# Kernel tuning notes

Measured on AMD Instinct MI355X. Metric: run time of the kernel, lower is better.

The kernel has to match this reference:

```python
import jax, jax.numpy as jnp
import numpy as np
from jax import lax

DIM, HEADS, DIM_HEAD = 768, 12, 64
INNER = HEADS * DIM_HEAD
DIM_ROT = 32
FH = FW = 32
N = 1 + FH * FW
B = 8


def setup_inputs() -> dict:
    key = jax.random.key(0)
    ks = jax.random.split(key, 8)
    s = 0.02
    return {
        "x": jax.random.normal(ks[0], (B, N, DIM), jnp.float32),
        "sin": jax.random.normal(ks[1], (N - 1, DIM_ROT), jnp.float32),
        "cos": jax.random.normal(ks[2], (N - 1, DIM_ROT), jnp.float32),
        "ln_g": jnp.ones((DIM,), jnp.float32),
        "ln_b": jnp.zeros((DIM,), jnp.float32),
        "dw_w": jax.random.normal(ks[3], (DIM, 1, 5, 5), jnp.float32) * s,
        "pw_w": jax.random.normal(ks[4], (INNER, DIM, 1, 1), jnp.float32) * s,
        "kv_w": jax.random.normal(ks[5], (DIM, 2 * INNER), jnp.float32) * s,
        "out_w": jax.random.normal(ks[6], (INNER, DIM), jnp.float32) * s,
        "out_b": jnp.zeros((DIM,), jnp.float32),
        "fmap_h": FH,
        "fmap_w": FW,
    }


def _rotate_every_two(t):
    # (..., d) with pairs (x1, x2) -> (-x2, x1)
    shp = t.shape
    t = t.reshape(*shp[:-1], -1, 2)
    x1, x2 = t[..., 0], t[..., 1]
    return jnp.stack((-x2, x1), axis=-1).reshape(shp)


def _layernorm(x, g, b, eps=1e-5):
    mu = jnp.mean(x, -1, keepdims=True)
    var = jnp.var(x, -1, keepdims=True)
    return (x - mu) * lax.rsqrt(var + eps) * g + b


def reference(x, sin, cos, ln_g, ln_b, dw_w, pw_w, kv_w, out_w, out_b, fmap_h, fmap_w):
    b, n, _ = x.shape
    scale = DIM_HEAD ** -0.5
    xn = _layernorm(x, ln_g, ln_b)

    # --- query path: SpatialConv (depthwise 5x5 + 1x1), cls via Identity ---
    cls_tok, spatial = xn[:, :1], xn[:, 1:]
    fmap = spatial.reshape(b, fmap_h, fmap_w, DIM).transpose(0, 3, 1, 2)  # NCHW
    fmap = lax.conv_general_dilated(
        fmap, dw_w, window_strides=(1, 1), padding=[(2, 2), (2, 2)],
        dimension_numbers=("NCHW", "OIHW", "NCHW"), feature_group_count=DIM)
    fmap = lax.conv_general_dilated(
        fmap, pw_w, window_strides=(1, 1), padding="VALID",
        dimension_numbers=("NCHW", "OIHW", "NCHW"))
    q = fmap.transpose(0, 2, 3, 1).reshape(b, fmap_h * fmap_w, INNER)
    q = jnp.concatenate((cls_tok, q), axis=1)  # cls_proj is Identity (dim==inner)

    # --- kv projection ---
    kv = xn @ kv_w
    k, v = kv[..., :INNER], kv[..., INNER:]

    def to_heads(t):  # b n (h d) -> (b h) n d
        return t.reshape(b, n, HEADS, DIM_HEAD).transpose(0, 2, 1, 3).reshape(b * HEADS, n, DIM_HEAD)

    q, k, v = map(to_heads, (q, k, v))

    # --- partial rotary, skipping cls token ---
    def apply_rot(t):
        t_cls, t_sp = t[:, :1], t[:, 1:]
        t_rot, t_pass = t_sp[..., :DIM_ROT], t_sp[..., DIM_ROT:]
        t_rot = t_rot * cos + _rotate_every_two(t_rot) * sin
        return jnp.concatenate((t_cls, jnp.concatenate((t_rot, t_pass), -1)), axis=1)

    q, k = apply_rot(q), apply_rot(k)

    dots = jnp.einsum("bid,bjd->bij", q, k) * scale
    attn = jax.nn.softmax(dots, axis=-1)
    out = jnp.einsum("bij,bjd->bid", attn, v)
    out = out.reshape(b, HEADS, n, DIM_HEAD).transpose(0, 2, 1, 3).reshape(b, n, INNER)
    return out @ out_w + out_b
```

## Files before the change

kernel.cpp:

```cpp
#include <hip/hip_runtime.h>
#include <cstddef>

#define NSEQ   1025
#define NBATCH 8
#define NTOK   8200
#define DIMX   768
#define NHEADS 12
#define DHEAD  64
#define VTP    1040
#define LDP    72
#define CP     136

typedef short bf16x8 __attribute__((ext_vector_type(8)));
typedef float f32x4  __attribute__((ext_vector_type(4)));
typedef unsigned short u16;

__device__ __forceinline__ float bf2f(u16 u) {
    unsigned v = (unsigned)u << 16; float f; __builtin_memcpy(&f, &v, 4); return f;
}
__device__ __forceinline__ u16 f2bf(float f) {
    unsigned u; __builtin_memcpy(&u, &f, 4);
    return (u16)((u + 0x7FFFu + ((u >> 16) & 1u)) >> 16);
}

__device__ __forceinline__ void gl2lds16(const u16* g, u16* l) {
    __builtin_amdgcn_global_load_lds((__attribute__((address_space(1))) void*)g,
                                     (__attribute__((address_space(3))) void*)l, 16, 0, 0);
}

__launch_bounds__(256)
__global__ void ln_kernel(const float* __restrict__ x, const float* __restrict__ g,
                          const float* __restrict__ bb, u16* __restrict__ xn,
                          u16* __restrict__ qout)
{
    int t = blockIdx.x, tid = threadIdx.x;
    const float* xp = x + (size_t)t * DIMX;
    float v0 = xp[tid], v1 = xp[tid + 256], v2 = xp[tid + 512];
    float s  = v0 + v1 + v2;
    float ss = v0*v0 + v1*v1 + v2*v2;
    for (int off = 32; off > 0; off >>= 1) {
        s  += __shfl_down(s,  off, 64);
        ss += __shfl_down(ss, off, 64);
    }
    __shared__ float red[8];
    __shared__ float stats[2];
    int w = tid >> 6, lane = tid & 63;
    if (lane == 0) { red[w] = s; red[4 + w] = ss; }
    __syncthreads();
    if (tid == 0) {
        float S  = red[0] + red[1] + red[2] + red[3];
        float SS = red[4] + red[5] + red[6] + red[7];
        float mu  = S * (1.0f / DIMX);
        float var = SS * (1.0f / DIMX) - mu * mu;
        stats[0] = mu; stats[1] = rsqrtf(var + 1e-5f);
    }
    __syncthreads();
    float mu = stats[0], rs = stats[1];
    u16 o0 = f2bf((v0 - mu) * rs * g[tid]       + bb[tid]);
    u16 o1 = f2bf((v1 - mu) * rs * g[tid + 256] + bb[tid + 256]);
    u16 o2 = f2bf((v2 - mu) * rs * g[tid + 512] + bb[tid + 512]);
    u16* op = xn + (size_t)t * DIMX;
    op[tid] = o0; op[tid + 256] = o1; op[tid + 512] = o2;
    int bq = t / NSEQ;
    if (t == bq * NSEQ) {
        int c0 = tid, c1 = tid + 256, c2 = tid + 512;
        qout[((size_t)(bq * NHEADS + (c0 >> 6)) * NSEQ) * DHEAD + (c0 & 63)] = o0;
        qout[((size_t)(bq * NHEADS + (c1 >> 6)) * NSEQ) * DHEAD + (c1 & 63)] = o1;
        qout[((size_t)(bq * NHEADS + (c2 >> 6)) * NSEQ) * DHEAD + (c2 & 63)] = o2;
    }
}

__launch_bounds__(256)
__global__ void preproc_kernel(const float* __restrict__ dw_w, const float* __restrict__ pw_w,
                               const float* __restrict__ kv_w, const float* __restrict__ out_w,
                               float* __restrict__ dwT, u16* __restrict__ pw_bf,
                               u16* __restrict__ kv_wT, u16* __restrict__ out_wT)
{
    __shared__ float tile[32][33];
    int blk = blockIdx.x, tid = threadIdx.x;
    if (blk < 75) {
        int idx = blk * 256 + tid;
        if (idx < 768 * 25) {
            int c = idx / 25, wi = idx % 25;
            dwT[wi * 768 + c] = dw_w[idx];
        }
        return;
    }
    if (blk < 2379) {
        int i = (blk - 75) * 256 + tid;
        pw_bf[i] = f2bf(pw_w[i]);
        return;
    }
    const float* in; u16* out; int R, C, bx, by;
    if (blk < 3531) {
        int t2 = blk - 2379; bx = t2 % 48; by = t2 / 48;
        in = kv_w; out = kv_wT; R = 768; C = 1536;
    } else {
        int t2 = blk - 3531; bx = t2 % 24; by = t2 / 24;
        in = out_w; out = out_wT; R = 768; C = 768;
    }
    int tx = tid & 31, ty = tid >> 5;
    int xg = bx * 32 + tx, y0 = by * 32;
    for (int i = ty; i < 32; i += 8)
        tile[i][tx] = in[(size_t)(y0 + i) * C + xg];
    __syncthreads();
    int xo = by * 32 + tx, yo0 = bx * 32;
    for (int i = ty; i < 32; i += 8)
        out[(size_t)(yo0 + i) * R + xo] = f2bf(tile[tx][i]);
}

__launch_bounds__(256)
__global__ void dw_kernel(const u16* __restrict__ xn, const float* __restrict__ wt,
                          u16* __restrict__ out)
{
    int gid = blockIdx.x * 256 + threadIdx.x;
    int pix = gid / 96, cg = gid - pix * 96;
    int c = cg * 8;
    int b = pix >> 10, p = pix & 1023, y = p >> 5, x0 = p & 31;
    float acc[8] = {};
    for (int dy = 0; dy < 5; dy++) {
        int yy = y + dy - 2;
        if ((unsigned)yy >= 32u) continue;
        for (int dx = 0; dx < 5; dx++) {
            int xx = x0 + dx - 2;
            if ((unsigned)xx >= 32u) continue;
            const u16* ip = xn + ((size_t)(b * NSEQ) + 1 + yy * 32 + xx) * DIMX + c;
            uint4 iv = *(const uint4*)ip;
            const float* wp = wt + (dy * 5 + dx) * DIMX + c;
            float4 w0 = *(const float4*)wp;
            float4 w1 = *(const float4*)(wp + 4);
            acc[0] += bf2f((u16)(iv.x & 0xFFFFu)) * w0.x;
            acc[1] += bf2f((u16)(iv.x >> 16))     * w0.y;
            acc[2] += bf2f((u16)(iv.y & 0xFFFFu)) * w0.z;
            acc[3] += bf2f((u16)(iv.y >> 16))     * w0.w;
            acc[4] += bf2f((u16)(iv.z & 0xFFFFu)) * w1.x;
            acc[5] += bf2f((u16)(iv.z >> 16))     * w1.y;
            acc[6] += bf2f((u16)(iv.w & 0xFFFFu)) * w1.z;
            acc[7] += bf2f((u16)(iv.w >> 16))     * w1.w;
        }
    }
    uint4 ov;
    ov.x = (unsigned)f2bf(acc[0]) | ((unsigned)f2bf(acc[1]) << 16);
    ov.y = (unsigned)f2bf(acc[2]) | ((unsigned)f2bf(acc[3]) << 16);
    ov.z = (unsigned)f2bf(acc[4]) | ((unsigned)f2bf(acc[5]) << 16);
    ov.w = (unsigned)f2bf(acc[6]) | ((unsigned)f2bf(acc[7]) << 16);
    *(uint4*)(out + (size_t)pix * DIMX + c) = ov;
}

template<int MODE>
__launch_bounds__(256)
__global__ void gemm_bf16(const u16* __restrict__ A, const u16* __restrict__ Bn,
                          const float* __restrict__ bias, u16* __restrict__ Ob0,
                          u16* __restrict__ Ob1, float* __restrict__ Of, int M)
{
    __shared__ u16 smem[128 * CP];
    u16* As = smem;
    u16* Bs = smem + 8192;
    const int tid  = threadIdx.x;
    const int wave = tid >> 6, lane = tid & 63;
    const int q8 = lane >> 4, cc = lane & 15;
    const int wr = wave >> 1, wc = wave & 1;
    const long r0 = (long)blockIdx.y * 128;
    const int  c0 = blockIdx.x * 128;

    f32x4 acc[4][4] = {};

    for (int k0 = 0; k0 < 768; k0 += 64) {
        __syncthreads();
        #pragma unroll
        for (int p = 0; p < 4; p++) {
            int chunk = wave * 256 + p * 64 + lane;
            int row = chunk >> 3, cs = chunk & 7;
            int src = cs ^ (row & 7);
            const u16* ga = A  + (size_t)(r0 + row) * 768 + k0 + src * 8;
            const u16* gb = Bn + (size_t)(c0 + row) * 768 + k0 + src * 8;
            u16* la = As + (size_t)(wave * 256 + p * 64) * 8;
            u16* lb = Bs + (size_t)(wave * 256 + p * 64) * 8;
            gl2lds16(ga, la);
            gl2lds16(gb, lb);
        }
        __syncthreads();
        #pragma unroll
        for (int ks = 0; ks < 2; ks++) {
            const int chsw = (((ks * 4 + q8) ^ (cc & 7)) * 8);
            bf16x8 af[4], bfr[4];
            #pragma unroll
            for (int mi = 0; mi < 4; mi++)
                af[mi] = *(const bf16x8*)(As + (wr * 64 + mi * 16 + cc) * 64 + chsw);
            #pragma unroll
            for (int ni = 0; ni < 4; ni++)
                bfr[ni] = *(const bf16x8*)(Bs + (wc * 64 + ni * 16 + cc) * 64 + chsw);
            #pragma unroll
            for (int mi = 0; mi < 4; mi++)
                #pragma unroll
                for (int ni = 0; ni < 4; ni++)
                    acc[mi][ni] = __builtin_amdgcn_mfma_f32_16x16x32_bf16(af[mi], bfr[ni], acc[mi][ni], 0, 0, 0);
        }
    }

    if (MODE == 2) {
        #pragma unroll
        for (int mi = 0; mi < 4; mi++) {
            #pragma unroll
            for (int r = 0; r < 4; r++) {
                long row = r0 + wr * 64 + mi * 16 + q8 * 4 + r;
                if (row >= M) continue;
                #pragma unroll
                for (int ni = 0; ni < 4; ni++) {
                    int col = c0 + wc * 64 + ni * 16 + cc;
                    Of[(size_t)row * 768 + col] = acc[mi][ni][r] + bias[col];
                }
            }
        }
        return;
    }

    __syncthreads();
    #pragma unroll
    for (int mi = 0; mi < 4; mi++)
        #pragma unroll
        for (int r = 0; r < 4; r++) {
            int lr = wr * 64 + mi * 16 + q8 * 4 + r;
            #pragma unroll
            for (int ni = 0; ni < 4; ni++)
                smem[lr * CP + wc * 64 + ni * 16 + cc] = f2bf(acc[mi][ni][r]);
        }
    __syncthreads();
    #pragma unroll
    for (int p = 0; p < 8; p++) {
        int id = p * 256 + tid;
        int row = id >> 4, c8 = (id & 15) * 8;
        long grow = r0 + row;
        if (grow >= M) continue;
        uint4 val = *(const uint4*)(smem + row * CP + c8);
        int b, n;
        if (MODE == 1) { b = (int)(grow >> 10); n = (int)(grow & 1023) + 1; }
        else           { b = (int)(grow / NSEQ); n = (int)(grow % NSEQ); }
        int col = c0 + c8;
        u16* dst; int c2;
        if (MODE == 0 && col >= 768) { dst = Ob1; c2 = col - 768; }
        else                         { dst = Ob0; c2 = col; }
        *(uint4*)(dst + ((size_t)(b * NHEADS + (c2 >> 6)) * NSEQ + n) * DHEAD + (c2 & 63)) = val;
    }
}

__launch_bounds__(256)
__global__ void rope_kernel(u16* __restrict__ q, u16* __restrict__ k,
                            const float* __restrict__ sinb, const float* __restrict__ cosb)
{
    int idx = blockIdx.x * 256 + threadIdx.x;
    int pr  = idx & 15;
    int pos = (idx >> 4) & 1023;
    int bh  = idx >> 14;
    float c0 = cosb[pos * 32 + pr * 2], c1 = cosb[pos * 32 + pr * 2 + 1];
    float s0 = sinb[pos * 32 + pr * 2], s1 = sinb[pos * 32 + pr * 2 + 1];
    size_t base = ((size_t)bh * NSEQ + 1 + pos) * DHEAD + pr * 2;
    float q0 = bf2f(q[base]), q1 = bf2f(q[base + 1]);
    float k0 = bf2f(k[base]), k1 = bf2f(k[base + 1]);
    q[base]     = f2bf(q0 * c0 - q1 * s0);
    q[base + 1] = f2bf(q1 * c1 + q0 * s1);
    k[base]     = f2bf(k0 * c0 - k1 * s0);
    k[base + 1] = f2bf(k1 * c1 + k0 * s1);
}

__global__ void vt_kernel(const u16* __restrict__ v, u16* __restrict__ Vt)
{
    __shared__ u16 tile[32][33];
    int bh = blockIdx.z;
    int n0 = blockIdx.x * 32, d0 = blockIdx.y * 32;
    for (int i = threadIdx.y; i < 32; i += 8) {
        int n = n0 + i;
        tile[i][threadIdx.x] = (n < NSEQ) ? v[((size_t)bh * NSEQ + n) * 64 + d0 + threadIdx.x] : (u16)0;
    }
    __syncthreads();
    for (int i = threadIdx.y; i < 32; i += 8) {
        int n = n0 + threadIdx.x;
        if (n < VTP) Vt[((size_t)bh * 64 + d0 + i) * VTP + n] = tile[threadIdx.x][i];
    }
}

__launch_bounds__(256)
__global__ void attn_kernel(const u16* __restrict__ q, const u16* __restrict__ k,
                            const u16* __restrict__ Vt, u16* __restrict__ o)
{
    __shared__ u16 Qs[64 * LDP];
    __shared__ u16 Ks[64 * LDP];
    __shared__ u16 Vs[64 * LDP];
    __shared__ u16 Ps[4 * 16 * LDP];
    const int tid  = threadIdx.x;
    const int wave = tid >> 6, lane = tid & 63;
    const int q8 = lane >> 4, cc = lane & 15;
    const int bh = blockIdx.x;
    const int i0 = blockIdx.y * 64;
    const int b = bh / NHEADS, h = bh % NHEADS;
    const size_t kqbase = (size_t)bh * NSEQ * 64;
    const size_t vtbase = (size_t)bh * 64 * VTP;

    #pragma unroll
    for (int pass = 0; pass < 2; pass++) {
        int ci = tid + pass * 256;
        int row = ci >> 3, ch = ci & 7;
        uint4 val = make_uint4(0, 0, 0, 0);
        if (i0 + row < NSEQ) val = *(const uint4*)(q + kqbase + (size_t)(i0 + row) * 64 + ch * 8);
        *(uint4*)(Qs + row * LDP + ch * 8) = val;
    }

    f32x4 O[4] = {};
    float lsum[4] = {0.f, 0.f, 0.f, 0.f};
    u16* Psw = Ps + wave * 16 * LDP;

    auto tile_body = [&](int j0, bool MASK) {
        __syncthreads();
        #pragma unroll
        for (int pass = 0; pass < 2; pass++) {
            int ci = tid + pass * 256;
            int row = ci >> 3, ch = ci & 7;
            uint4 kv4 = make_uint4(0, 0, 0, 0);
            if (j0 + row < NSEQ) kv4 = *(const uint4*)(k + kqbase + (size_t)(j0 + row) * 64 + ch * 8);
            *(uint4*)(Ks + row * LDP + ch * 8) = kv4;
            uint4 vv4 = make_uint4(0, 0, 0, 0);
            if (j0 + ch * 8 < VTP) vv4 = *(const uint4*)(Vt + vtbase + (size_t)row * VTP + j0 + ch * 8);
            *(uint4*)(Vs + row * LDP + ch * 8) = vv4;
        }
        __syncthreads();

        f32x4 sf[4] = {};
        #pragma unroll
        for (int ks = 0; ks < 2; ks++) {
            bf16x8 aq = *(const bf16x8*)(Qs + (wave * 16 + cc) * LDP + ks * 32 + q8 * 8);
            #pragma unroll
            for (int ni = 0; ni < 4; ni++) {
                bf16x8 bk = *(const bf16x8*)(Ks + (ni * 16 + cc) * LDP + ks * 32 + q8 * 8);
                sf[ni] = __builtin_amdgcn_mfma_f32_16x16x32_bf16(aq, bk, sf[ni], 0, 0, 0);
            }
        }

        #pragma unroll
        for (int ni = 0; ni < 4; ni++) {
            #pragma unroll
            for (int r = 0; r < 4; r++) {
                float p = __expf(sf[ni][r] * 0.125f);
                if (MASK && (j0 + ni * 16 + cc >= NSEQ)) p = 0.f;
                lsum[r] += p;
                unsigned u; __builtin_memcpy(&u, &p, 4);
                Psw[(q8 * 4 + r) * LDP + ni * 16 + cc] = (u16)((u + 0x8000u) >> 16);
            }
        }

        #pragma unroll
        for (int ks = 0; ks < 2; ks++) {
            bf16x8 pa = *(const bf16x8*)(Psw + cc * LDP + ks * 32 + q8 * 8);
            #pragma unroll
            for (int ni = 0; ni < 4; ni++) {
                bf16x8 vb = *(const bf16x8*)(Vs + (ni * 16 + cc) * LDP + ks * 32 + q8 * 8);
                O[ni] = __builtin_amdgcn_mfma_f32_16x16x32_bf16(pa, vb, O[ni], 0, 0, 0);
            }
        }
    };

    for (int jt = 0; jt < 16; jt++) tile_body(jt * 64, false);
    tile_body(1024, true);

    #pragma unroll
    for (int r = 0; r < 4; r++) {
        lsum[r] += __shfl_xor(lsum[r], 1, 64);
        lsum[r] += __shfl_xor(lsum[r], 2, 64);
        lsum[r] += __shfl_xor(lsum[r], 4, 64);
        lsum[r] += __shfl_xor(lsum[r], 8, 64);
    }
    #pragma unroll
    for (int r = 0; r < 4; r++) {
        int i = i0 + wave * 16 + q8 * 4 + r;
        if (i >= NSEQ) continue;
        float inv = 1.0f / lsum[r];
        #pragma unroll
        for (int ni = 0; ni < 4; ni++)
            o[((size_t)(b * NSEQ + i)) * 768 + h * 64 + ni * 16 + cc] = f2bf(O[ni][r] * inv);
    }
}

extern "C" void kernel_launch(void* const* d_in, const int* in_sizes, int n_in,
                              void* d_out, int out_size, void* d_ws, size_t ws_size,
                              hipStream_t stream)
{
    const float* x     = (const float*)d_in[0];
    const float* sinb  = (const float*)d_in[1];
    const float* cosb  = (const float*)d_in[2];
    const float* ln_g  = (const float*)d_in[3];
    const float* ln_b  = (const float*)d_in[4];
    const float* dw_w  = (const float*)d_in[5];
    const float* pw_w  = (const float*)d_in[6];
    const float* kv_w  = (const float*)d_in[7];
    const float* out_w = (const float*)d_in[8];
    const float* out_b = (const float*)d_in[9];
    (void)in_sizes; (void)n_in; (void)out_size; (void)ws_size;

    u16* ws = (u16*)d_ws;
    u16* xn_bf    = ws;
    u16* dwout_bf = ws + 6297600;
    u16* q_bf     = ws + 12589056;
    u16* k_bf     = ws + 18886656;
    u16* v_bf     = ws + 25184256;
    u16* Vt       = ws + 31481856;
    u16* pw_bf    = ws + 37871616;
    u16* kv_wT    = ws + 38461440;
    u16* out_wT   = ws + 39641088;
    float* dwT    = (float*)(ws + 40230912);
    u16* attn_bf  = xn_bf;

    ln_kernel      <<<NTOK, 256, 0, stream>>>(x, ln_g, ln_b, xn_bf, q_bf);
    preproc_kernel <<<4107, 256, 0, stream>>>(dw_w, pw_w, kv_w, out_w, dwT, pw_bf, kv_wT, out_wT);
    dw_kernel      <<<3072, 256, 0, stream>>>(xn_bf, dwT, dwout_bf);
    gemm_bf16<1>   <<<dim3(6, 64), 256, 0, stream>>>(dwout_bf, pw_bf, nullptr, q_bf, nullptr, nullptr, 8192);
    gemm_bf16<0>   <<<dim3(12, 65), 256, 0, stream>>>(xn_bf, kv_wT, nullptr, k_bf, v_bf, nullptr, NTOK);
    rope_kernel    <<<6144, 256, 0, stream>>>(q_bf, k_bf, sinb, cosb);
    vt_kernel      <<<dim3(33, 2, 96), dim3(32, 8), 0, stream>>>(v_bf, Vt);
    attn_kernel    <<<dim3(96, 17), 256, 0, stream>>>(q_bf, k_bf, Vt, attn_bf);
    gemm_bf16<2>   <<<dim3(6, 65), 256, 0, stream>>>(attn_bf, out_wT, out_b, nullptr, nullptr, (float*)d_out, NTOK);
}
```

Before: 306.4 us.

## Fuse RoPE and softmax scale into GEMM epilogue; double-buffer attention K/V loads

Removes the separate rope kernel by applying rotary embedding to q and k in the projection GEMM epilogue. The 1/sqrt(d) scale is folded into q (in layernorm for the cls row and in the GEMM epilogue for spatial rows), so attention no longer multiplies scores. The attention kernel now keeps Q in registers, stages K/V into double-buffered swizzled LDS through direct global-to-LDS loads, and prefetches the next tile while computing the current one. The K/V staging drops its bounds checks, so the last tile reads past the sequence end and depends on masking and padding. Rounding q to bf16 after scaling by a power of two does not change precision.

```diff
diff --git a/kernel.cpp b/kernel.cpp
--- a/kernel.cpp
+++ b/kernel.cpp
@@ -56,17 +56,17 @@
     }
     __syncthreads();
     float mu = stats[0], rs = stats[1];
-    u16 o0 = f2bf((v0 - mu) * rs * g[tid]       + bb[tid]);
-    u16 o1 = f2bf((v1 - mu) * rs * g[tid + 256] + bb[tid + 256]);
-    u16 o2 = f2bf((v2 - mu) * rs * g[tid + 512] + bb[tid + 512]);
+    float y0 = (v0 - mu) * rs * g[tid]       + bb[tid];
+    float y1 = (v1 - mu) * rs * g[tid + 256] + bb[tid + 256];
+    float y2 = (v2 - mu) * rs * g[tid + 512] + bb[tid + 512];
     u16* op = xn + (size_t)t * DIMX;
-    op[tid] = o0; op[tid + 256] = o1; op[tid + 512] = o2;
+    op[tid] = f2bf(y0); op[tid + 256] = f2bf(y1); op[tid + 512] = f2bf(y2);
     int bq = t / NSEQ;
     if (t == bq * NSEQ) {
         int c0 = tid, c1 = tid + 256, c2 = tid + 512;
-        qout[((size_t)(bq * NHEADS + (c0 >> 6)) * NSEQ) * DHEAD + (c0 & 63)] = o0;
-        qout[((size_t)(bq * NHEADS + (c1 >> 6)) * NSEQ) * DHEAD + (c1 & 63)] = o1;
-        qout[((size_t)(bq * NHEADS + (c2 >> 6)) * NSEQ) * DHEAD + (c2 & 63)] = o2;
+        qout[((size_t)(bq * NHEADS + (c0 >> 6)) * NSEQ) * DHEAD + (c0 & 63)] = f2bf(y0 * 0.125f);
+        qout[((size_t)(bq * NHEADS + (c1 >> 6)) * NSEQ) * DHEAD + (c1 & 63)] = f2bf(y1 * 0.125f);
+        qout[((size_t)(bq * NHEADS + (c2 >> 6)) * NSEQ) * DHEAD + (c2 & 63)] = f2bf(y2 * 0.125f);
     }
 }
 
@@ -151,7 +151,9 @@
 __launch_bounds__(256)
 __global__ void gemm_bf16(const u16* __restrict__ A, const u16* __restrict__ Bn,
                           const float* __restrict__ bias, u16* __restrict__ Ob0,
-                          u16* __restrict__ Ob1, float* __restrict__ Of, int M)
+                          u16* __restrict__ Ob1, float* __restrict__ Of,
+                          const float* __restrict__ sinb, const float* __restrict__ cosb,
+                          int M)
 {
     __shared__ u16 smem[128 * CP];
     u16* As = smem;
@@ -238,29 +240,48 @@
         else           { b = (int)(grow / NSEQ); n = (int)(grow % NSEQ); }
         int col = c0 + c8;
         u16* dst; int c2;
-        if (MODE == 0 && col >= 768) { dst = Ob1; c2 = col - 768; }
-        else                         { dst = Ob0; c2 = col; }
+        bool isV = (MODE == 0 && col >= 768);
+        if (isV) { dst = Ob1; c2 = col - 768; }
+        else     { dst = Ob0; c2 = col; }
+        int d0 = c2 & 63;
+        if (!isV) {
+            u16 e[8];
+            unsigned wv[4] = {val.x, val.y, val.z, val.w};
+            #pragma unroll
+            for (int j = 0; j < 4; j++) { e[2*j] = (u16)(wv[j] & 0xFFFFu); e[2*j+1] = (u16)(wv[j] >> 16); }
+            bool doro = (d0 < 32) && (n >= 1);
+            if (MODE == 1 || doro) {
+                float f[8];
+                #pragma unroll
+                for (int j = 0; j < 8; j++) f[j] = bf2f(e[j]);
+                if (MODE == 1) {
+                    #pragma unroll
+                    for (int j = 0; j < 8; j++) f[j] *= 0.125f;
+                }
+                if (doro) {
+                    int pos = n - 1;
+                    const float* cp = cosb + pos * 32 + d0;
+                    const float* sp = sinb + pos * 32 + d0;
+                    float4 cv0 = *(const float4*)cp, cv1 = *(const float4*)(cp + 4);
+                    float4 sv0 = *(const float4*)sp, sv1 = *(const float4*)(sp + 4);
+                    float ca[8] = {cv0.x, cv0.y, cv0.z, cv0.w, cv1.x, cv1.y, cv1.z, cv1.w};
+                    float sa[8] = {sv0.x, sv0.y, sv0.z, sv0.w, sv1.x, sv1.y, sv1.z, sv1.w};
+                    #pragma unroll
+                    for (int pr = 0; pr < 4; pr++) {
+                        float a = f[2*pr], bb2 = f[2*pr+1];
+                        f[2*pr]   = a   * ca[2*pr]   - bb2 * sa[2*pr];
+                        f[2*pr+1] = bb2 * ca[2*pr+1] + a   * sa[2*pr+1];
+                    }
+                }
+                #pragma unroll
+                for (int j = 0; j < 8; j++) e[j] = f2bf(f[j]);
+            }
+            #pragma unroll
+            for (int j = 0; j < 4; j++) wv[j] = (unsigned)e[2*j] | ((unsigned)e[2*j+1] << 16);
+            val = make_uint4(wv[0], wv[1], wv[2], wv[3]);
+        }
         *(uint4*)(dst + ((size_t)(b * NHEADS + (c2 >> 6)) * NSEQ + n) * DHEAD + (c2 & 63)) = val;
     }
-}
-
-__launch_bounds__(256)
-__global__ void rope_kernel(u16* __restrict__ q, u16* __restrict__ k,
-                            const float* __restrict__ sinb, const float* __restrict__ cosb)
-{
-    int idx = blockIdx.x * 256 + threadIdx.x;
-    int pr  = idx & 15;
-    int pos = (idx >> 4) & 1023;
-    int bh  = idx >> 14;
-    float c0 = cosb[pos * 32 + pr * 2], c1 = cosb[pos * 32 + pr * 2 + 1];
-    float s0 = sinb[pos * 32 + pr * 2], s1 = sinb[pos * 32 + pr * 2 + 1];
-    size_t base = ((size_t)bh * NSEQ + 1 + pos) * DHEAD + pr * 2;
-    float q0 = bf2f(q[base]), q1 = bf2f(q[base + 1]);
-    float k0 = bf2f(k[base]), k1 = bf2f(k[base + 1]);
-    q[base]     = f2bf(q0 * c0 - q1 * s0);
-    q[base + 1] = f2bf(q1 * c1 + q0 * s1);
-    k[base]     = f2bf(k0 * c0 - k1 * s0);
-    k[base + 1] = f2bf(k1 * c1 + k0 * s1);
 }
 
 __global__ void vt_kernel(const u16* __restrict__ v, u16* __restrict__ Vt)
@@ -283,9 +304,8 @@
 __global__ void attn_kernel(const u16* __restrict__ q, const u16* __restrict__ k,
                             const u16* __restrict__ Vt, u16* __restrict__ o)
 {
-    __shared__ u16 Qs[64 * LDP];
-    __shared__ u16 Ks[64 * LDP];
-    __shared__ u16 Vs[64 * LDP];
+    __shared__ u16 Kb[2][64 * 64];
+    __shared__ u16 Vb[2][64 * 64];
     __shared__ u16 Ps[4 * 16 * LDP];
     const int tid  = threadIdx.x;
     const int wave = tid >> 6, lane = tid & 63;
@@ -293,54 +313,58 @@
     const int bh = blockIdx.x;
     const int i0 = blockIdx.y * 64;
     const int b = bh / NHEADS, h = bh % NHEADS;
-    const size_t kqbase = (size_t)bh * NSEQ * 64;
+    const size_t kbase  = (size_t)bh * NSEQ * 64;
     const size_t vtbase = (size_t)bh * 64 * VTP;
 
-    #pragma unroll
-    for (int pass = 0; pass < 2; pass++) {
-        int ci = tid + pass * 256;
-        int row = ci >> 3, ch = ci & 7;
-        uint4 val = make_uint4(0, 0, 0, 0);
-        if (i0 + row < NSEQ) val = *(const uint4*)(q + kqbase + (size_t)(i0 + row) * 64 + ch * 8);
-        *(uint4*)(Qs + row * LDP + ch * 8) = val;
-    }
-
+    bf16x8 aq[2];
+    {
+        const u16* qp = q + kbase + (size_t)(i0 + wave * 16 + cc) * 64;
+        aq[0] = *(const bf16x8*)(qp + q8 * 8);
+        aq[1] = *(const bf16x8*)(qp + 32 + q8 * 8);
+    }
+
+    auto stage = [&](int jt, int buf) {
+        int j0 = jt * 64;
+        #pragma unroll
+        for (int p = 0; p < 2; p++) {
+            int chunk = wave * 128 + p * 64 + lane;
+            int row = chunk >> 3, cs = chunk & 7;
+            int src = cs ^ (row & 7);
+            u16* kd = Kb[buf] + (size_t)(wave * 128 + p * 64) * 8;
+            u16* vd = Vb[buf] + (size_t)(wave * 128 + p * 64) * 8;
+            gl2lds16(k  + kbase  + (size_t)(j0 + row) * 64 + src * 8, kd);
+            gl2lds16(Vt + vtbase + (size_t)row * VTP + j0 + src * 8, vd);
+        }
+    };
+
+    stage(0, 0);
     f32x4 O[4] = {};
     float lsum[4] = {0.f, 0.f, 0.f, 0.f};
     u16* Psw = Ps + wave * 16 * LDP;
 
-    auto tile_body = [&](int j0, bool MASK) {
+    for (int jt = 0; jt < 17; jt++) {
         __syncthreads();
-        #pragma unroll
-        for (int pass = 0; pass < 2; pass++) {
-            int ci = tid + pass * 256;
-            int row = ci >> 3, ch = ci & 7;
-            uint4 kv4 = make_uint4(0, 0, 0, 0);
-            if (j0 + row < NSEQ) kv4 = *(const uint4*)(k + kqbase + (size_t)(j0 + row) * 64 + ch * 8);
-            *(uint4*)(Ks + row * LDP + ch * 8) = kv4;
-            uint4 vv4 = make_uint4(0, 0, 0, 0);
-            if (j0 + ch * 8 < VTP) vv4 = *(const uint4*)(Vt + vtbase + (size_t)row * VTP + j0 + ch * 8);
-            *(uint4*)(Vs + row * LDP + ch * 8) = vv4;
-        }
-        __syncthreads();
+        const u16* Kc = Kb[jt & 1];
+        const u16* Vc = Vb[jt & 1];
+        if (jt < 16) stage(jt + 1, (jt + 1) & 1);
 
         f32x4 sf[4] = {};
         #pragma unroll
         for (int ks = 0; ks < 2; ks++) {
-            bf16x8 aq = *(const bf16x8*)(Qs + (wave * 16 + cc) * LDP + ks * 32 + q8 * 8);
             #pragma unroll
             for (int ni = 0; ni < 4; ni++) {
-                bf16x8 bk = *(const bf16x8*)(Ks + (ni * 16 + cc) * LDP + ks * 32 + q8 * 8);
-                sf[ni] = __builtin_amdgcn_mfma_f32_16x16x32_bf16(aq, bk, sf[ni], 0, 0, 0);
+                bf16x8 bk = *(const bf16x8*)(Kc + (ni * 16 + cc) * 64 + (((ks * 4 + q8) ^ (cc & 7)) * 8));
+                sf[ni] = __builtin_amdgcn_mfma_f32_16x16x32_bf16(aq[ks], bk, sf[ni], 0, 0, 0);
             }
         }
 
+        bool mask = (jt == 16);
         #pragma unroll
         for (int ni = 0; ni < 4; ni++) {
             #pragma unroll
             for (int r = 0; r < 4; r++) {
-                float p = __expf(sf[ni][r] * 0.125f);
-                if (MASK && (j0 + ni * 16 + cc >= NSEQ)) p = 0.f;
+                float p = __expf(sf[ni][r]);
+                if (mask && (1024 + ni * 16 + cc >= NSEQ)) p = 0.f;
                 lsum[r] += p;
                 unsigned u; __builtin_memcpy(&u, &p, 4);
                 Psw[(q8 * 4 + r) * LDP + ni * 16 + cc] = (u16)((u + 0x8000u) >> 16);
@@ -352,14 +376,11 @@
             bf16x8 pa = *(const bf16x8*)(Psw + cc * LDP + ks * 32 + q8 * 8);
             #pragma unroll
             for (int ni = 0; ni < 4; ni++) {
-                bf16x8 vb = *(const bf16x8*)(Vs + (ni * 16 + cc) * LDP + ks * 32 + q8 * 8);
+                bf16x8 vb = *(const bf16x8*)(Vc + (ni * 16 + cc) * 64 + (((ks * 4 + q8) ^ (cc & 7)) * 8));
                 O[ni] = __builtin_amdgcn_mfma_f32_16x16x32_bf16(pa, vb, O[ni], 0, 0, 0);
             }
         }
-    };
-
-    for (int jt = 0; jt < 16; jt++) tile_body(jt * 64, false);
-    tile_body(1024, true);
+    }
 
     #pragma unroll
     for (int r = 0; r < 4; r++) {
@@ -411,10 +432,9 @@
     ln_kernel      <<<NTOK, 256, 0, stream>>>(x, ln_g, ln_b, xn_bf, q_bf);
     preproc_kernel <<<4107, 256, 0, stream>>>(dw_w, pw_w, kv_w, out_w, dwT, pw_bf, kv_wT, out_wT);
     dw_kernel      <<<3072, 256, 0, stream>>>(xn_bf, dwT, dwout_bf);
-    gemm_bf16<1>   <<<dim3(6, 64), 256, 0, stream>>>(dwout_bf, pw_bf, nullptr, q_bf, nullptr, nullptr, 8192);
-    gemm_bf16<0>   <<<dim3(12, 65), 256, 0, stream>>>(xn_bf, kv_wT, nullptr, k_bf, v_bf, nullptr, NTOK);
-    rope_kernel    <<<6144, 256, 0, stream>>>(q_bf, k_bf, sinb, cosb);
+    gemm_bf16<1>   <<<dim3(6, 64), 256, 0, stream>>>(dwout_bf, pw_bf, nullptr, q_bf, nullptr, nullptr, sinb, cosb, 8192);
+    gemm_bf16<0>   <<<dim3(12, 65), 256, 0, stream>>>(xn_bf, kv_wT, nullptr, k_bf, v_bf, nullptr, sinb, cosb, NTOK);
     vt_kernel      <<<dim3(33, 2, 96), dim3(32, 8), 0, stream>>>(v_bf, Vt);
     attn_kernel    <<<dim3(96, 17), 256, 0, stream>>>(q_bf, k_bf, Vt, attn_bf);
-    gemm_bf16<2>   <<<dim3(6, 65), 256, 0, stream>>>(attn_bf, out_wT, out_b, nullptr, nullptr, (float*)d_out, NTOK);
-}
+    gemm_bf16<2>   <<<dim3(6, 65), 256, 0, stream>>>(attn_bf, out_wT, out_b, nullptr, nullptr, (float*)d_out, nullptr, nullptr, NTOK);
+}
```

Result: no change. 306.7 us (+0.1%).
